# Kernel tuning notes

Measured on AMD Instinct MI355X. Metric: run time of the kernel, lower is better.

The kernel has to match this reference:

```python
import jax, jax.numpy as jnp
import numpy as np

B, Q, KV = 2, 2048, 2048
D_MODEL = 1024
N_HEADS = 16
D_KV = 64
EPS = 1e-6


def setup_inputs() -> dict:
    key = jax.random.key(0)
    ks = jax.random.split(key, 7)
    s = 0.02
    return {
        "hidden_states": jax.random.normal(ks[0], (B, Q, D_MODEL), jnp.float32),
        "key_value_states": jax.random.normal(ks[1], (B, KV, D_MODEL), jnp.float32),
        "wq": jax.random.normal(ks[2], (D_MODEL, N_HEADS * D_KV), jnp.float32) * s,
        "wk": jax.random.normal(ks[3], (D_MODEL, N_HEADS * D_KV), jnp.float32) * s,
        "wv": jax.random.normal(ks[4], (D_MODEL, N_HEADS * D_KV), jnp.float32) * s,
        "wo": jax.random.normal(ks[5], (N_HEADS * D_KV, D_MODEL), jnp.float32) * s,
        "norm_w": jnp.ones((D_MODEL,), jnp.float32),
    }


def reference(hidden_states, key_value_states, wq, wk, wv, wo, norm_w):
    # RMSNorm (T5-style, no mean subtraction)
    var = jnp.mean(jnp.square(hidden_states), axis=-1, keepdims=True)
    normed = hidden_states * jax.lax.rsqrt(var + EPS) * norm_w

    b, q_len, _ = hidden_states.shape
    kv_len = key_value_states.shape[1]

    def split_heads(x):  # [b, s, H*d] -> [b, H, s, d]
        return x.reshape(b, -1, N_HEADS, D_KV).transpose(0, 2, 1, 3)

    q = split_heads(normed @ wq)              # [b,H,q,d]
    k = split_heads(key_value_states @ wk)    # [b,H,kv,d]
    v = split_heads(key_value_states @ wv)    # [b,H,kv,d]

    # T5 attention: NO 1/sqrt(d) scaling; position_bias is zeros here
    # (has_relative_attention_bias=False, no mask) so it is a no-op.
    scores = jnp.einsum("bhqd,bhkd->bhqk", q, k)
    attn = jax.nn.softmax(scores.astype(jnp.float32), axis=-1).astype(scores.dtype)
    ctx = jnp.einsum("bhqk,bhkd->bhqd", attn, v)
    ctx = ctx.transpose(0, 2, 1, 3).reshape(b, q_len, N_HEADS * D_KV)
    attn_out = ctx @ wo

    # residual connection
    return hidden_states + attn_out
```

## Files before the change

### kernel.cpp

```cpp
#include <hip/hip_runtime.h>


typedef __attribute__((ext_vector_type(8)))  short s16x8;
typedef __attribute__((ext_vector_type(4)))  float f32x4;
typedef __attribute__((ext_vector_type(16))) float f32x16;
typedef __attribute__((ext_vector_type(4)))  int   i32x4;

#define LOG2E 1.4426950408889634f
#define EXP2(x) __builtin_amdgcn_exp2f(x)

__device__ __forceinline__ unsigned short f2bf(float f) {
  unsigned int u = __builtin_bit_cast(unsigned int, f);
  return (unsigned short)((u + 0x7FFFu + ((u >> 16) & 1u)) >> 16);
}

__device__ __forceinline__ unsigned cvtpk(float lo, float hi) {
  unsigned r;
  asm("v_cvt_pk_bf16_f32 %0, %1, %2" : "=v"(r) : "v"(lo), "v"(hi));
  return r;
}

__device__ __forceinline__ float f3max(float a, float b, float c) {
  return fmaxf(fmaxf(a, b), c);
}

__device__ __forceinline__ void gload16(const void* g, void* l) {
  __builtin_amdgcn_global_load_lds(
      (const __attribute__((address_space(1))) unsigned int*)g,
      (__attribute__((address_space(3))) unsigned int*)l, 16, 0, 0);
}

__global__ __launch_bounds__(256) void k_transpose4(
    const float* __restrict__ a0, const float* __restrict__ a1,
    const float* __restrict__ a2, const float* __restrict__ a3,
    unsigned short* __restrict__ o0, unsigned short* __restrict__ o1,
    unsigned short* __restrict__ o2, unsigned short* __restrict__ o3) {
  int z = blockIdx.z;
  const float* in = (z == 0) ? a0 : (z == 1) ? a1 : (z == 2) ? a2 : a3;
  unsigned short* out = (z == 0) ? o0 : (z == 1) ? o1 : (z == 2) ? o2 : o3;
  __shared__ float tile[64][65];
  int t = threadIdx.x;
  int tx = t & 15, ty = t >> 4;
  int r0 = blockIdx.y * 64, c0 = blockIdx.x * 64;
#pragma unroll
  for (int p = 0; p < 4; ++p) {
    int r = p * 16 + ty;
    float4 v = *reinterpret_cast<const float4*>(in + (size_t)(r0 + r) * 1024 + c0 + tx * 4);
    tile[r][tx * 4 + 0] = v.x; tile[r][tx * 4 + 1] = v.y;
    tile[r][tx * 4 + 2] = v.z; tile[r][tx * 4 + 3] = v.w;
  }
  __syncthreads();
#pragma unroll
  for (int p = 0; p < 4; ++p) {
    int c = p * 16 + ty;
    unsigned int lo = (unsigned int)f2bf(tile[tx * 4 + 0][c]) |
                      ((unsigned int)f2bf(tile[tx * 4 + 1][c]) << 16);
    unsigned int hi = (unsigned int)f2bf(tile[tx * 4 + 2][c]) |
                      ((unsigned int)f2bf(tile[tx * 4 + 3][c]) << 16);
    uint2 pk2; pk2.x = lo; pk2.y = hi;
    *reinterpret_cast<uint2*>(out + (size_t)(c0 + c) * 1024 + r0 + tx * 4) = pk2;
  }
}

__global__ __launch_bounds__(256) void k_prep(
    const float* __restrict__ hs, const float* __restrict__ w,
    unsigned short* __restrict__ normed,
    const float* __restrict__ kvs, unsigned short* __restrict__ kvb) {
  int t = threadIdx.x;
  if (blockIdx.x < 4096) {
    int row = blockIdx.x;
    float4 v = *reinterpret_cast<const float4*>(hs + (size_t)row * 1024 + t * 4);
    float s = v.x * v.x + v.y * v.y + v.z * v.z + v.w * v.w;
#pragma unroll
    for (int m = 1; m < 64; m <<= 1) s += __shfl_xor(s, m);
    __shared__ float ps[4];
    if ((t & 63) == 0) ps[t >> 6] = s;
    __syncthreads();
    float tot = ps[0] + ps[1] + ps[2] + ps[3];
    float sc = rsqrtf(tot * (1.0f / 1024.0f) + 1e-6f) * LOG2E;
    float4 wv = *reinterpret_cast<const float4*>(w + t * 4);
    unsigned int lo = (unsigned int)f2bf(v.x * sc * wv.x) |
                      ((unsigned int)f2bf(v.y * sc * wv.y) << 16);
    unsigned int hi = (unsigned int)f2bf(v.z * sc * wv.z) |
                      ((unsigned int)f2bf(v.w * sc * wv.w) << 16);
    uint2 pk2; pk2.x = lo; pk2.y = hi;
    *reinterpret_cast<uint2*>(normed + (size_t)row * 1024 + t * 4) = pk2;
  } else {
    int i = (blockIdx.x - 4096) * 256 + t;
    for (; i < 1048576; i += 1024 * 256) {
      float4 v = *reinterpret_cast<const float4*>(kvs + (size_t)i * 4);
      unsigned int lo = (unsigned int)f2bf(v.x) | ((unsigned int)f2bf(v.y) << 16);
      unsigned int hi = (unsigned int)f2bf(v.z) | ((unsigned int)f2bf(v.w) << 16);
      uint2 pk2; pk2.x = lo; pk2.y = hi;
      *reinterpret_cast<uint2*>(kvb + (size_t)i * 4) = pk2;
    }
  }
}

template <int BM>
__device__ __forceinline__ void gemm_body(
    const unsigned short* __restrict__ A, const unsigned short* __restrict__ Bt,
    void* __restrict__ Cout, const float* __restrict__ resid, int mode) {
  constexpr int MF = BM / 32;
  constexpr int ATILE = BM * 128;
  __shared__ __align__(16) char sm[2 * ATILE + 32768];
  int t = threadIdx.x;
  int bn = blockIdx.x, bm = blockIdx.y;
  int m0 = bm * BM, n0 = bn * 128;
  int lane = t & 63, w = t >> 6, lr = lane & 15, lg = lane >> 4;
  int wr = w >> 1, wc = w & 1;

  f32x4 acc[MF][4] = {};

  const char* aA = (const char*)A + ((size_t)(m0 + (t >> 3)) * 1024 + (t & 7) * 8) * 2;
  const char* aB = (const char*)Bt + ((size_t)(n0 + (t >> 3)) * 1024 + (t & 7) * 8) * 2;

  auto stage = [&](int buf, int kt) {
    int koff = kt * 128;
    char* As = sm + buf * ATILE;
    char* Bs = sm + 2 * ATILE + buf * 16384;
#pragma unroll
    for (int c = 0; c < BM / 32; ++c)
      gload16(aA + (size_t)c * 65536 + koff, As + c * 4096 + t * 16);
#pragma unroll
    for (int c = 0; c < 4; ++c)
      gload16(aB + (size_t)c * 65536 + koff, Bs + c * 4096 + t * 16);
  };

  stage(0, 0);
  __syncthreads();
  int cur = 0;
  for (int kt = 0; kt < 16; ++kt) {
    if (kt < 15) stage(cur ^ 1, kt + 1);
    const char* As = sm + cur * ATILE;
    const char* Bs = sm + 2 * ATILE + cur * 16384;
    s16x8 af[2][MF], bfr[2][4];
#pragma unroll
    for (int ks = 0; ks < 2; ++ks) {
#pragma unroll
      for (int m = 0; m < MF; ++m)
        af[ks][m] = *reinterpret_cast<const s16x8*>(
            As + (wr * (BM / 2) + m * 16 + lr) * 128 + ks * 64 + lg * 16);
#pragma unroll
      for (int n = 0; n < 4; ++n)
        bfr[ks][n] = *reinterpret_cast<const s16x8*>(
            Bs + (wc * 64 + n * 16 + lr) * 128 + ks * 64 + lg * 16);
    }
#pragma unroll
    for (int ks = 0; ks < 2; ++ks)
#pragma unroll
      for (int m = 0; m < MF; ++m)
#pragma unroll
        for (int n = 0; n < 4; ++n)
          acc[m][n] = __builtin_amdgcn_mfma_f32_16x16x32_bf16(af[ks][m], bfr[ks][n], acc[m][n], 0, 0, 0);
    __syncthreads();
    cur ^= 1;
  }

#pragma unroll
  for (int m = 0; m < MF; ++m)
#pragma unroll
    for (int n = 0; n < 4; ++n) {
      int colg = n0 + wc * 64 + n * 16 + lr;
      int rowb = m0 + wr * (BM / 2) + m * 16 + lg * 4;
      if (mode == 0) {
        unsigned short* C = (unsigned short*)Cout;
#pragma unroll
        for (int r = 0; r < 4; ++r)
          C[(size_t)(rowb + r) * 1024 + colg] = f2bf(acc[m][n][r]);
      } else if (mode == 1) {
        int h = colg >> 6, d = colg & 63;
        int b = rowb >> 11, kv = rowb & 2047;
        unsigned short* C = (unsigned short*)Cout +
            ((size_t)((b * 16 + h) * 64 + d) * 2048 + kv);
        unsigned int lo = (unsigned int)f2bf(acc[m][n][0]) |
                          ((unsigned int)f2bf(acc[m][n][1]) << 16);
        unsigned int hi = (unsigned int)f2bf(acc[m][n][2]) |
                          ((unsigned int)f2bf(acc[m][n][3]) << 16);
        uint2 pk2; pk2.x = lo; pk2.y = hi;
        *reinterpret_cast<uint2*>(C) = pk2;
      } else {
        float* C = (float*)Cout;
#pragma unroll
        for (int r = 0; r < 4; ++r) {
          size_t idx = (size_t)(rowb + r) * 1024 + colg;
          C[idx] = resid[idx] + acc[m][n][r];
        }
      }
    }
}

__global__ __launch_bounds__(256) void k_gemm_qkv(
    const unsigned short* __restrict__ normed, const unsigned short* __restrict__ kvb,
    const unsigned short* __restrict__ wqT, const unsigned short* __restrict__ wkT,
    const unsigned short* __restrict__ wvT,
    unsigned short* __restrict__ qb, unsigned short* __restrict__ kb,
    unsigned short* __restrict__ vTb) {
  int z = blockIdx.z;
  const unsigned short* A = (z == 0) ? normed : kvb;
  const unsigned short* B = (z == 0) ? wqT : (z == 1) ? wkT : wvT;
  void* C = (z == 0) ? (void*)qb : (z == 1) ? (void*)kb : (void*)vTb;
  gemm_body<128>(A, B, C, nullptr, (z == 2) ? 1 : 0);
}

__global__ __launch_bounds__(256) void k_gemm_o(
    const unsigned short* __restrict__ ctxb, const unsigned short* __restrict__ woT,
    float* __restrict__ out, const float* __restrict__ hs) {
  gemm_body<64>(ctxb, woT, (void*)out, hs, 2);
}

__global__ __launch_bounds__(256, 2) void k_attn(
    const unsigned short* __restrict__ q, const unsigned short* __restrict__ k,
    const unsigned short* __restrict__ vt, unsigned short* __restrict__ ctx) {
  __shared__ __align__(16) char sm[65536];
  int t = threadIdx.x, w = t >> 6, lane = t & 63;
  int l5 = lane & 31, hi = lane >> 5, l7 = lane & 7;

  int bid = blockIdx.x;
  int xcd = bid & 7, slot = bid >> 3;
  int bh = xcd * 4 + (slot >> 4);
  int qt = slot & 15;
  int b = bh >> 4, h = bh & 15;

  const char* qB = (const char*)q + ((size_t)(b * 2048 + qt * 128) * 1024 + h * 64) * 2;
  const char* kB = (const char*)k + ((size_t)(b * 2048) * 1024 + h * 64) * 2;
  const char* vB = (const char*)vt + (size_t)bh * 64 * 4096;

  int krow = t >> 3;
  int kcb  = ((t & 7) * 16) ^ ((krow & 7) << 4);
  int vrow = t >> 4;
  int vcb  = ((t & 15) * 16) ^ ((vrow & 7) << 4);

  auto stageKV = [&](int buf, int it2) {
    char* Kd = sm + buf * 16384;
    char* Vd = sm + 32768 + buf * 16384;
    const char* kb2 = kB + (size_t)(it2 * 128) * 2048;
    const char* vb2 = vB + it2 * 256;
#pragma unroll
    for (int c = 0; c < 4; ++c) {
      gload16(kb2 + (size_t)(c * 32 + krow) * 2048 + kcb, Kd + c * 4096 + t * 16);
      gload16(vb2 + (size_t)(c * 16 + vrow) * 4096 + vcb, Vd + c * 4096 + t * 16);
    }
  };

#pragma unroll
  for (int c = 0; c < 4; ++c)
    gload16(qB + (size_t)(c * 32 + krow) * 2048 + kcb, sm + c * 4096 + t * 16);
  __syncthreads();
  s16x8 qa[4];
#pragma unroll
  for (int s = 0; s < 4; ++s) {
    int row = w * 32 + l5;
    qa[s] = *reinterpret_cast<const s16x8*>(
        sm + row * 128 + ((32 * s + 16 * hi) ^ (l7 << 4)));
  }
  __syncthreads();
  stageKV(0, 0);
  stageKV(1, 1);

  f32x16 octx[2] = {};
  float mrun = -1e30f;
  float lsum = 0.0f;

  for (int it = 0; it < 16; ++it) {
    if (it < 14) {
      asm volatile("s_waitcnt vmcnt(8)" ::: "memory");
    } else {
      asm volatile("s_waitcnt vmcnt(0)" ::: "memory");
    }
    __builtin_amdgcn_s_barrier();
    __builtin_amdgcn_sched_barrier(0);

    const char* Ks = sm + (it & 1) * 16384;
    const char* Vs = sm + 32768 + (it & 1) * 16384;

#pragma unroll
    for (int hh = 0; hh < 2; ++hh) {
      f32x16 s2[2] = {};
      __builtin_amdgcn_s_setprio(1);
#pragma unroll
      for (int kb = 0; kb < 2; ++kb) {
        int kvb = hh * 2 + kb;
#pragma unroll
        for (int s = 0; s < 4; ++s) {
          s16x8 ka = *reinterpret_cast<const s16x8*>(
              Ks + (kvb * 32 + l5) * 128 + ((32 * s + 16 * hi) ^ (l7 << 4)));
          s2[kb] = __builtin_amdgcn_mfma_f32_32x32x16_bf16(ka, qa[s], s2[kb], 0, 0, 0);
        }
      }
      __builtin_amdgcn_s_setprio(0);

      float m2 = -1e30f;
#pragma unroll
      for (int kb = 0; kb < 2; ++kb)
#pragma unroll
        for (int r = 0; r < 16; r += 2)
          m2 = f3max(m2, s2[kb][r], s2[kb][r + 1]);
      m2 = fmaxf(m2, __shfl_xor(m2, 32));
      if (__any(m2 > mrun + 8.0f)) {
        float mx = fmaxf(mrun, m2);
        float sc = EXP2(mrun - mx);
        mrun = mx;
        lsum *= sc;
#pragma unroll
        for (int r = 0; r < 16; ++r) {
          float scr = __shfl(sc, (r & 3) + 8 * (r >> 2) + 4 * hi);
          octx[0][r] *= scr;
          octx[1][r] *= scr;
        }
      }

#pragma unroll
      for (int kb = 0; kb < 2; ++kb) {
        int kvb = hh * 2 + kb;
        float p[16];
        float a0 = 0.0f, a1 = 0.0f;
#pragma unroll
        for (int r = 0; r < 16; r += 2) {
          p[r]     = EXP2(s2[kb][r] - mrun);
          p[r + 1] = EXP2(s2[kb][r + 1] - mrun);
          a0 += p[r]; a1 += p[r + 1];
        }
        lsum += a0 + a1;
        i32x4 pf[2];
#pragma unroll
        for (int s = 0; s < 2; ++s) {
          pf[s][0] = (int)cvtpk(p[8 * s + 0], p[8 * s + 1]);
          pf[s][1] = (int)cvtpk(p[8 * s + 2], p[8 * s + 3]);
          pf[s][2] = (int)cvtpk(p[8 * s + 4], p[8 * s + 5]);
          pf[s][3] = (int)cvtpk(p[8 * s + 6], p[8 * s + 7]);
        }
        __builtin_amdgcn_s_setprio(1);
#pragma unroll
        for (int dt = 0; dt < 2; ++dt) {
          int row = dt * 32 + l5;
          const char* vbase = Vs + row * 256;
#pragma unroll
          for (int s = 0; s < 2; ++s) {
            int coff = 64 * kvb + 32 * s + 8 * hi;
            uint2 v1 = *reinterpret_cast<const uint2*>(vbase + (coff ^ (l7 << 4)));
            uint2 v2 = *reinterpret_cast<const uint2*>(vbase + ((coff + 16) ^ (l7 << 4)));
            i32x4 vv; vv[0] = (int)v1.x; vv[1] = (int)v1.y;
            vv[2] = (int)v2.x; vv[3] = (int)v2.y;
            octx[dt] = __builtin_amdgcn_mfma_f32_32x32x16_bf16(
                __builtin_bit_cast(s16x8, pf[s]),
                __builtin_bit_cast(s16x8, vv), octx[dt], 0, 0, 0);
          }
        }
        __builtin_amdgcn_s_setprio(0);
      }
    }

    __builtin_amdgcn_s_barrier();
    __builtin_amdgcn_sched_barrier(0);
    if (it < 14) stageKV(it & 1, it + 2);
  }

  {
    float tot = lsum + __shfl_xor(lsum, 32);
    float inv = 1.0f / tot;
#pragma unroll
    for (int r = 0; r < 16; ++r) {
      int qrow = (r & 3) + 8 * (r >> 2) + 4 * hi;
      float invr = __shfl(inv, qrow);
      int grow = qt * 128 + w * 32 + qrow;
#pragma unroll
      for (int dt = 0; dt < 2; ++dt)
        ctx[(size_t)(b * 2048 + grow) * 1024 + h * 64 + dt * 32 + l5] =
            f2bf(octx[dt][r] * invr);
    }
  }
}

extern "C" void kernel_launch(void* const* d_in, const int* in_sizes, int n_in,
                              void* d_out, int out_size, void* d_ws, size_t ws_size,
                              hipStream_t stream) {
  const float* hs  = (const float*)d_in[0];
  const float* kvs = (const float*)d_in[1];
  const float* wq  = (const float*)d_in[2];
  const float* wk  = (const float*)d_in[3];
  const float* wv  = (const float*)d_in[4];
  const float* wo  = (const float*)d_in[5];
  const float* nw  = (const float*)d_in[6];
  float* out = (float*)d_out;
  char* ws = (char*)d_ws;

  unsigned short* normed = (unsigned short*)(ws + (size_t)0);
  unsigned short* kvb    = (unsigned short*)(ws + ((size_t)8 << 20));
  unsigned short* wqT    = (unsigned short*)(ws + ((size_t)16 << 20));
  unsigned short* wkT    = (unsigned short*)(ws + ((size_t)18 << 20));
  unsigned short* wvT    = (unsigned short*)(ws + ((size_t)20 << 20));
  unsigned short* woT    = (unsigned short*)(ws + ((size_t)22 << 20));
  unsigned short* qb     = (unsigned short*)(ws + ((size_t)24 << 20));
  unsigned short* kb     = (unsigned short*)(ws + ((size_t)32 << 20));
  unsigned short* vTb    = (unsigned short*)(ws + ((size_t)40 << 20));
  unsigned short* ctxb   = (unsigned short*)(ws + ((size_t)48 << 20));

  k_transpose4<<<dim3(16, 16, 4), 256, 0, stream>>>(wq, wk, wv, wo, wqT, wkT, wvT, woT);
  k_prep<<<5120, 256, 0, stream>>>(hs, nw, normed, kvs, kvb);

  k_gemm_qkv<<<dim3(8, 32, 3), 256, 0, stream>>>(normed, kvb, wqT, wkT, wvT, qb, kb, vTb);

  k_attn<<<512, 256, 0, stream>>>(qb, kb, vTb, ctxb);

  k_gemm_o<<<dim3(8, 64), 256, 0, stream>>>(ctxb, woT, out, hs);
}
```

Baseline: 138.0 us.

## Halve GEMM K-tile and use explicit vmcnt waits with split barriers

The GEMM main loop now uses a 64-wide K tile with 32 iterations instead of a 128-wide tile with 16. Both shared-memory buffers are prefetched up front, and each iteration waits on a vmcnt count so the next stage's loads stay in flight. MFMA issue priority is raised with s_setprio, and launch bounds now request 4 blocks per CU to raise occupancy. The halved shared memory and finer pipeline aim to overlap global loads with compute better. The cost is more barriers per K, and it assumes gload16 is an async direct-to-LDS load so that the vmcnt counts are correct.

```diff
diff --git a/kernel.cpp b/kernel.cpp
--- a/kernel.cpp
+++ b/kernel.cpp
@@ -102,8 +102,10 @@
     const unsigned short* __restrict__ A, const unsigned short* __restrict__ Bt,
     void* __restrict__ Cout, const float* __restrict__ resid, int mode) {
   constexpr int MF = BM / 32;
-  constexpr int ATILE = BM * 128;
-  __shared__ __align__(16) char sm[2 * ATILE + 32768];
+  constexpr int AROUNDS = BM / 64;
+  constexpr int ATILE = BM * 64;
+  constexpr int LPS = AROUNDS + 2;
+  __shared__ __align__(16) char sm[2 * ATILE + 16384];
   int t = threadIdx.x;
   int bn = blockIdx.x, bm = blockIdx.y;
   int m0 = bm * BM, n0 = bn * 128;
@@ -112,49 +114,54 @@
 
   f32x4 acc[MF][4] = {};
 
-  const char* aA = (const char*)A + ((size_t)(m0 + (t >> 3)) * 1024 + (t & 7) * 8) * 2;
-  const char* aB = (const char*)Bt + ((size_t)(n0 + (t >> 3)) * 1024 + (t & 7) * 8) * 2;
+  const char* aA = (const char*)A + ((size_t)(m0 + (t >> 2)) * 1024 + (t & 3) * 8) * 2;
+  const char* aB = (const char*)Bt + ((size_t)(n0 + (t >> 2)) * 1024 + (t & 3) * 8) * 2;
 
   auto stage = [&](int buf, int kt) {
-    int koff = kt * 128;
+    int koff = kt * 64;
     char* As = sm + buf * ATILE;
-    char* Bs = sm + 2 * ATILE + buf * 16384;
-#pragma unroll
-    for (int c = 0; c < BM / 32; ++c)
-      gload16(aA + (size_t)c * 65536 + koff, As + c * 4096 + t * 16);
-#pragma unroll
-    for (int c = 0; c < 4; ++c)
-      gload16(aB + (size_t)c * 65536 + koff, Bs + c * 4096 + t * 16);
+    char* Bs = sm + 2 * ATILE + buf * 8192;
+#pragma unroll
+    for (int c = 0; c < AROUNDS; ++c)
+      gload16(aA + (size_t)c * 131072 + koff, As + c * 4096 + t * 16);
+#pragma unroll
+    for (int c = 0; c < 2; ++c)
+      gload16(aB + (size_t)c * 131072 + koff, Bs + c * 4096 + t * 16);
   };
 
   stage(0, 0);
-  __syncthreads();
-  int cur = 0;
-  for (int kt = 0; kt < 16; ++kt) {
-    if (kt < 15) stage(cur ^ 1, kt + 1);
-    const char* As = sm + cur * ATILE;
-    const char* Bs = sm + 2 * ATILE + cur * 16384;
-    s16x8 af[2][MF], bfr[2][4];
-#pragma unroll
-    for (int ks = 0; ks < 2; ++ks) {
-#pragma unroll
-      for (int m = 0; m < MF; ++m)
-        af[ks][m] = *reinterpret_cast<const s16x8*>(
-            As + (wr * (BM / 2) + m * 16 + lr) * 128 + ks * 64 + lg * 16);
+  stage(1, 1);
+  for (int kt = 0; kt < 32; ++kt) {
+    if (kt < 31) {
+      asm volatile("s_waitcnt vmcnt(%0)" :: "i"(LPS) : "memory");
+    } else {
+      asm volatile("s_waitcnt vmcnt(0)" ::: "memory");
+    }
+    __builtin_amdgcn_s_barrier();
+    __builtin_amdgcn_sched_barrier(0);
+
+    const char* As = sm + (kt & 1) * ATILE;
+    const char* Bs = sm + 2 * ATILE + (kt & 1) * 8192;
+    s16x8 af[MF], bfr[4];
+#pragma unroll
+    for (int m = 0; m < MF; ++m)
+      af[m] = *reinterpret_cast<const s16x8*>(
+          As + (wr * (BM / 2) + m * 16 + lr) * 64 + lg * 16);
+#pragma unroll
+    for (int n = 0; n < 4; ++n)
+      bfr[n] = *reinterpret_cast<const s16x8*>(
+          Bs + (wc * 64 + n * 16 + lr) * 64 + lg * 16);
+    __builtin_amdgcn_s_setprio(1);
+#pragma unroll
+    for (int m = 0; m < MF; ++m)
 #pragma unroll
       for (int n = 0; n < 4; ++n)
-        bfr[ks][n] = *reinterpret_cast<const s16x8*>(
-            Bs + (wc * 64 + n * 16 + lr) * 128 + ks * 64 + lg * 16);
-    }
-#pragma unroll
-    for (int ks = 0; ks < 2; ++ks)
-#pragma unroll
-      for (int m = 0; m < MF; ++m)
-#pragma unroll
-        for (int n = 0; n < 4; ++n)
-          acc[m][n] = __builtin_amdgcn_mfma_f32_16x16x32_bf16(af[ks][m], bfr[ks][n], acc[m][n], 0, 0, 0);
-    __syncthreads();
-    cur ^= 1;
+        acc[m][n] = __builtin_amdgcn_mfma_f32_16x16x32_bf16(af[m], bfr[n], acc[m][n], 0, 0, 0);
+    __builtin_amdgcn_s_setprio(0);
+
+    __builtin_amdgcn_s_barrier();
+    __builtin_amdgcn_sched_barrier(0);
+    if (kt < 30) stage(kt & 1, kt + 2);
   }
 
 #pragma unroll
@@ -190,7 +197,7 @@
     }
 }
 
-__global__ __launch_bounds__(256) void k_gemm_qkv(
+__global__ __launch_bounds__(256, 4) void k_gemm_qkv(
     const unsigned short* __restrict__ normed, const unsigned short* __restrict__ kvb,
     const unsigned short* __restrict__ wqT, const unsigned short* __restrict__ wkT,
     const unsigned short* __restrict__ wvT,
@@ -203,7 +210,7 @@
   gemm_body<128>(A, B, C, nullptr, (z == 2) ? 1 : 0);
 }
 
-__global__ __launch_bounds__(256) void k_gemm_o(
+__global__ __launch_bounds__(256, 4) void k_gemm_o(
     const unsigned short* __restrict__ ctxb, const unsigned short* __restrict__ woT,
     float* __restrict__ out, const float* __restrict__ hs) {
   gemm_body<64>(ctxb, woT, (void*)out, hs, 2);
```

After: 134.9 us. -2.2%, faster.
